# Kernel tuning notes

Hardware: AMD Instinct MI355X
Metric: run time of the kernel (lower is better)

Reference implementation:

```python
import jax, jax.numpy as jnp
import numpy as np

D_MODEL = 1024
N_HEADS = 16
N_KV_HEADS = 4
HEAD_DIM = 64


def setup_inputs() -> dict:
    key = jax.random.key(0)
    ks = jax.random.split(key, 5)
    B, T, P = 2, 512, 8
    scale = 1.0 / np.sqrt(D_MODEL)
    return {
        "hidden_states": jax.random.normal(ks[0], (B, T, P, D_MODEL), dtype=jnp.float32),
        # weights stored [in, out] so y = x @ W (same math as nn.Linear with W^T)
        "Wq": jax.random.normal(ks[1], (D_MODEL, N_HEADS * HEAD_DIM), dtype=jnp.float32) * scale,
        "Wk": jax.random.normal(ks[2], (D_MODEL, N_KV_HEADS * HEAD_DIM), dtype=jnp.float32) * scale,
        "Wv": jax.random.normal(ks[3], (D_MODEL, N_KV_HEADS * HEAD_DIM), dtype=jnp.float32) * scale,
        "Wo": jax.random.normal(ks[4], (N_HEADS * HEAD_DIM, D_MODEL), dtype=jnp.float32) * scale,
    }


def _rope_tables(T, d):
    half = d // 2
    inv_freq = 1.0 / (10000.0 ** (jnp.arange(half, dtype=jnp.float32) / half))
    pos = jnp.arange(T, dtype=jnp.float32)
    angles = pos[:, None] * inv_freq[None, :]  # (T, half)
    return jnp.cos(angles), jnp.sin(angles)


def _apply_rope(x, cos, sin):
    # x: (B, P, T, H, d); cos/sin: (T, d/2)
    half = x.shape[-1] // 2
    x1, x2 = x[..., :half], x[..., half:]
    c = cos[None, None, :, None, :]
    s = sin[None, None, :, None, :]
    return jnp.concatenate([x1 * c - x2 * s, x1 * s + x2 * c], axis=-1)


def reference(hidden_states, Wq, Wk, Wv, Wo):
    B, T, P, _ = hidden_states.shape
    x = jnp.transpose(hidden_states, (0, 2, 1, 3))  # (B, P, T, C)
    q = (x @ Wq).reshape(B, P, T, N_HEADS, HEAD_DIM)
    k = (x @ Wk).reshape(B, P, T, N_KV_HEADS, HEAD_DIM)
    v = (x @ Wv).reshape(B, P, T, N_KV_HEADS, HEAD_DIM)

    rep = N_HEADS // N_KV_HEADS
    k = jnp.repeat(k, rep, axis=3)  # (B,P,T,H,d) interleaved like torch repeat/view
    v = jnp.repeat(v, rep, axis=3)

    cos, sin = _rope_tables(T, HEAD_DIM)
    q = _apply_rope(q, cos, sin)
    k = _apply_rope(k, cos, sin)

    # (B,P,H,T,d)
    q = jnp.transpose(q, (0, 1, 3, 2, 4))
    k = jnp.transpose(k, (0, 1, 3, 2, 4))
    v = jnp.transpose(v, (0, 1, 3, 2, 4))

    attn = jnp.einsum("bphqd,bphkd->bphqk", q, k) / jnp.sqrt(
        jnp.asarray(HEAD_DIM, q.dtype))
    attn = jax.nn.softmax(attn, axis=-1)
    out = jnp.einsum("bphqk,bphkd->bphqd", attn, v)
    out = jnp.transpose(out, (0, 1, 3, 2, 4)).reshape(B, P, T, N_HEADS * HEAD_DIM)
    out = jnp.transpose(out, (0, 2, 1, 3))  # (B, T, P, H*d)
    return out @ Wo
```

## Files before the change

kernel.cpp:

```cpp
#include <hip/hip_runtime.h>
#include <stdint.h>


typedef __attribute__((ext_vector_type(8))) short bf16x8;
typedef __attribute__((ext_vector_type(4))) float f32x4;
typedef __attribute__((ext_vector_type(16))) float f32x16;
typedef __attribute__((ext_vector_type(4))) unsigned short us4;
typedef __attribute__((ext_vector_type(8))) unsigned short us8;

static __device__ __forceinline__ unsigned short f2bf(float f) {
  unsigned u = __float_as_uint(f);
  u += 0x7fffu + ((u >> 16) & 1u);
  return (unsigned short)(u >> 16);
}

static __device__ __forceinline__ void ld_lds16(const void* g, void* l) {
  __builtin_amdgcn_global_load_lds(
      (const __attribute__((address_space(1))) void*)g,
      (__attribute__((address_space(3))) void*)l, 16, 0, 0);
}

static __device__ __forceinline__ f32x4 mfma16(bf16x8 a, bf16x8 b, f32x4 c) {
  return __builtin_amdgcn_mfma_f32_16x16x32_bf16(a, b, c, 0, 0, 0);
}
static __device__ __forceinline__ f32x16 mfma32(bf16x8 a, bf16x8 b, f32x16 c) {
  return __builtin_amdgcn_mfma_f32_32x32x16_bf16(a, b, c, 0, 0, 0);
}

__global__ __launch_bounds__(256) void conv_all(
    const float* __restrict__ hs, const float* __restrict__ Wq,
    const float* __restrict__ Wk, const float* __restrict__ Wv,
    const float* __restrict__ Wo, unsigned short* __restrict__ xb,
    unsigned short* __restrict__ wqkv, unsigned short* __restrict__ wot) {
  __shared__ float tile[64][65];
  int bid = blockIdx.x, tid = threadIdx.x;
  if (bid < 8192) {
    int gid = bid * 256 + tid;
    size_t e = (size_t)gid * 4;
    int r = (int)(e >> 10);
    int d = (int)(e & 1023);
    int b = r >> 12, p = (r >> 9) & 7, t = r & 511;
    const float4* src = (const float4*)(hs + ((((size_t)b * 512 + t) * 8 + p) << 10) + d);
    float4 v = *src;
    us4 o;
    o.x = f2bf(v.x); o.y = f2bf(v.y); o.z = f2bf(v.z); o.w = f2bf(v.w);
    *(us4*)(xb + e) = o;
    return;
  }
  int tb = bid - 8192;
  const float* W; unsigned short* Wt; int N, tc0, tn0;
  if (tb < 256)      { W = Wq; Wt = wqkv;                       N = 1024; tc0 = (tb >> 4) * 64;          tn0 = (tb & 15) * 64; }
  else if (tb < 320) { W = Wk; Wt = wqkv + (size_t)1024 * 1024; N = 256;  tc0 = ((tb - 256) >> 2) * 64;  tn0 = ((tb - 256) & 3) * 64; }
  else if (tb < 384) { W = Wv; Wt = wqkv + (size_t)1280 * 1024; N = 256;  tc0 = ((tb - 320) >> 2) * 64;  tn0 = ((tb - 320) & 3) * 64; }
  else               { W = Wo; Wt = wot;                        N = 1024; tc0 = ((tb - 384) >> 4) * 64;  tn0 = ((tb - 384) & 15) * 64; }
  int tr = tid >> 4, tc = tid & 15;
#pragma unroll
  for (int i = 0; i < 4; ++i) {
    int c = tr + i * 16;
    float4 v = *(const float4*)(W + (size_t)(tc0 + c) * N + tn0 + tc * 4);
    tile[c][tc * 4 + 0] = v.x; tile[c][tc * 4 + 1] = v.y;
    tile[c][tc * 4 + 2] = v.z; tile[c][tc * 4 + 3] = v.w;
  }
  __syncthreads();
#pragma unroll
  for (int i = 0; i < 4; ++i) {
    int n = tr + i * 16;
    us4 o;
    o.x = f2bf(tile[tc * 4 + 0][n]); o.y = f2bf(tile[tc * 4 + 1][n]);
    o.z = f2bf(tile[tc * 4 + 2][n]); o.w = f2bf(tile[tc * 4 + 3][n]);
    *(us4*)(Wt + (size_t)(tn0 + n) * 1024 + tc0 + tc * 4) = o;
  }
}

__global__ __launch_bounds__(512, 2) void gemm_qkv(
    const unsigned short* __restrict__ A, const unsigned short* __restrict__ Bt,
    unsigned short* __restrict__ qb, unsigned short* __restrict__ kb,
    unsigned short* __restrict__ vtb) {
  constexpr int K = 1024;
  constexpr int KT = K / 64;
  __shared__ __align__(16) unsigned short Sm[2][2][256 * 64];
  unsigned short* Cs = &Sm[0][0][0];

  int tid = threadIdx.x;
  int lane = tid & 63, wid = tid >> 6;
  int quad = lane >> 4, lo = lane & 15;
  int wg = (blockIdx.x & 7) * 24 + (blockIdx.x >> 3);
  int tn = wg % 6, tm = wg / 6;
  int wr = wid >> 2, wc = wid & 3;
  int srow = lane >> 3, schunk = lane & 7;
  int cg = schunk ^ srow;

  const unsigned short* pa = A + ((size_t)(tm * 256) + wid * 8 + srow) * K + cg * 8;
  const unsigned short* pb = Bt + ((size_t)(tn * 256) + wid * 8 + srow) * K + cg * 8;

  f32x4 z = {0.f, 0.f, 0.f, 0.f};
  f32x4 acc[8][4];
#pragma unroll
  for (int i = 0; i < 8; ++i)
#pragma unroll
    for (int j = 0; j < 4; ++j) acc[i][j] = z;

  auto stage = [&](int t, int p) {
#pragma unroll
    for (int i = 0; i < 4; ++i) {
      ld_lds16(pa + (size_t)i * 64 * K + t * 64,
               (char*)&Sm[p][0][0] + (wid * 8 + i * 64) * 128);
      ld_lds16(pb + (size_t)i * 64 * K + t * 64,
               (char*)&Sm[p][1][0] + (wid * 8 + i * 64) * 128);
    }
  };

  stage(0, 0);
  stage(1, 1);
  asm volatile("s_waitcnt vmcnt(8)" ::: "memory");
  asm volatile("s_barrier" ::: "memory");

  bf16x8 af[4][2], bb0[2][2], bb1[2][2];

  for (int t = 0; t < KT; ++t) {
    int p = t & 1;
    const unsigned short* As = &Sm[p][0][0];
    const unsigned short* Bs = &Sm[p][1][0];

#pragma unroll
    for (int mi = 0; mi < 4; ++mi)
#pragma unroll
      for (int kx = 0; kx < 2; ++kx) {
        int row = wr * 128 + mi * 16 + lo;
        int cgx = (quad + kx * 4) ^ (row & 7);
        af[mi][kx] = *(const bf16x8*)(As + (size_t)row * 64 + cgx * 8);
      }
#pragma unroll
    for (int ni = 0; ni < 2; ++ni)
#pragma unroll
      for (int kx = 0; kx < 2; ++kx) {
        int row = wc * 64 + ni * 16 + lo;
        int cgx = (quad + kx * 4) ^ (row & 7);
        bb0[ni][kx] = *(const bf16x8*)(Bs + (size_t)row * 64 + cgx * 8);
      }
    asm volatile("s_barrier" ::: "memory");
    __builtin_amdgcn_s_setprio(1);
#pragma unroll
    for (int kx = 0; kx < 2; ++kx)
#pragma unroll
      for (int mi = 0; mi < 4; ++mi)
#pragma unroll
        for (int ni = 0; ni < 2; ++ni)
          acc[mi][ni] = mfma16(af[mi][kx], bb0[ni][kx], acc[mi][ni]);
    __builtin_amdgcn_s_setprio(0);
    asm volatile("s_barrier" ::: "memory");

#pragma unroll
    for (int ni = 0; ni < 2; ++ni)
#pragma unroll
      for (int kx = 0; kx < 2; ++kx) {
        int row = wc * 64 + (ni + 2) * 16 + lo;
        int cgx = (quad + kx * 4) ^ (row & 7);
        bb1[ni][kx] = *(const bf16x8*)(Bs + (size_t)row * 64 + cgx * 8);
      }
    asm volatile("s_barrier" ::: "memory");
    __builtin_amdgcn_s_setprio(1);
#pragma unroll
    for (int kx = 0; kx < 2; ++kx)
#pragma unroll
      for (int mi = 0; mi < 4; ++mi)
#pragma unroll
        for (int ni = 0; ni < 2; ++ni)
          acc[mi][ni + 2] = mfma16(af[mi][kx], bb1[ni][kx], acc[mi][ni + 2]);
    __builtin_amdgcn_s_setprio(0);
    asm volatile("s_barrier" ::: "memory");

#pragma unroll
    for (int mi = 0; mi < 4; ++mi)
#pragma unroll
      for (int kx = 0; kx < 2; ++kx) {
        int row = wr * 128 + 64 + mi * 16 + lo;
        int cgx = (quad + kx * 4) ^ (row & 7);
        af[mi][kx] = *(const bf16x8*)(As + (size_t)row * 64 + cgx * 8);
      }
    asm volatile("s_barrier" ::: "memory");
    __builtin_amdgcn_s_setprio(1);
#pragma unroll
    for (int kx = 0; kx < 2; ++kx)
#pragma unroll
      for (int mi = 0; mi < 4; ++mi)
#pragma unroll
        for (int ni = 0; ni < 2; ++ni)
          acc[mi + 4][ni + 2] = mfma16(af[mi][kx], bb1[ni][kx], acc[mi + 4][ni + 2]);
    __builtin_amdgcn_s_setprio(0);
    asm volatile("s_barrier" ::: "memory");

    bool pf = (t + 2 < KT);
    if (pf) stage(t + 2, p);
    __builtin_amdgcn_s_setprio(1);
#pragma unroll
    for (int kx = 0; kx < 2; ++kx)
#pragma unroll
      for (int mi = 0; mi < 4; ++mi)
#pragma unroll
        for (int ni = 0; ni < 2; ++ni)
          acc[mi + 4][ni] = mfma16(af[mi][kx], bb0[ni][kx], acc[mi + 4][ni]);
    __builtin_amdgcn_s_setprio(0);
    if (pf) asm volatile("s_waitcnt vmcnt(8)" ::: "memory");
    else    asm volatile("s_waitcnt vmcnt(0)" ::: "memory");
    asm volatile("s_barrier" ::: "memory");
  }

  if (tn < 5) {
    float qscale = (tn < 4) ? 0.125f : 1.0f;
#pragma unroll
    for (int mi = 0; mi < 8; ++mi)
#pragma unroll
      for (int r = 0; r < 4; ++r) {
        int row = wr * 128 + mi * 16 + quad * 4 + r;
        int tpos = (tm * 256 + row) & 511;
#pragma unroll
        for (int ni = 0; ni < 2; ++ni) {
          float invf = exp2f((float)(ni * 16 + lo) * -0.41524101186092029f);
          float ang = (float)tpos * invf;
          float s, c;
          __sincosf(ang, &s, &c);
          float x1 = acc[mi][ni][r], x2 = acc[mi][ni + 2][r];
          acc[mi][ni][r]     = (x1 * c - x2 * s) * qscale;
          acc[mi][ni + 2][r] = (x1 * s + x2 * c) * qscale;
        }
      }
#pragma unroll
    for (int mi = 0; mi < 8; ++mi)
#pragma unroll
      for (int ni = 0; ni < 4; ++ni)
#pragma unroll
        for (int r = 0; r < 4; ++r) {
          int row = wr * 128 + mi * 16 + quad * 4 + r;
          int col = wc * 64 + ni * 16 + lo;
          int cs = col ^ (((row >> 2) & 3) << 3);
          Cs[row * 256 + cs] = f2bf(acc[mi][ni][r]);
        }
    __syncthreads();
    int tc = tid & 31, ro = tid >> 5;
#pragma unroll
    for (int it = 0; it < 16; ++it) {
      int row = ro + 16 * it;
      int cs = (tc * 8) ^ (((row >> 2) & 3) << 3);
      us8 v = *(const us8*)(Cs + row * 256 + cs);
      size_t grow = (size_t)(tm * 256 + row);
      if (tn < 4) *(us8*)(qb + grow * 1024 + tn * 256 + tc * 8) = v;
      else        *(us8*)(kb + grow * 256 + tc * 8) = v;
    }
  } else {
#pragma unroll
    for (int mi = 0; mi < 8; ++mi)
#pragma unroll
      for (int ni = 0; ni < 4; ++ni)
#pragma unroll
        for (int r = 0; r < 4; ++r) {
          int trow = wr * 128 + mi * 16 + quad * 4 + r;
          int col = wc * 64 + ni * 16 + lo;
          Cs[col * 256 + (trow ^ ((col & 7) << 3))] = f2bf(acc[mi][ni][r]);
        }
    __syncthreads();
    int t0 = (tid & 31) * 8, colIdx = tid >> 5;
    int bp = tm >> 1, tbase = (tm & 1) * 256;
#pragma unroll
    for (int it = 0; it < 16; ++it) {
      int col = colIdx + it * 16;
      us8 v = *(const us8*)(Cs + col * 256 + (t0 ^ ((col & 7) << 3)));
      int hh = col >> 6, dd = col & 63;
      *(us8*)(vtb + (((size_t)(bp * 4 + hh)) * 64 + dd) * 512 + tbase + t0) = v;
    }
  }
}

__global__ __launch_bounds__(512, 2) void gemm_o(
    const unsigned short* __restrict__ A, const unsigned short* __restrict__ Bt,
    float* __restrict__ out) {
  constexpr int K = 1024;
  constexpr int KT = K / 64;
  __shared__ __align__(16) unsigned short Sm[2][(128 + 256) * 64];

  int tid = threadIdx.x;
  int lane = tid & 63, wid = tid >> 6;
  int quad = lane >> 4, lo = lane & 15;
  int wg = (blockIdx.x & 7) * 32 + (blockIdx.x >> 3);
  int tn = wg & 3, tm = wg >> 2;
  int wr = wid >> 2, wc = wid & 3;
  int srow = lane >> 3, schunk = lane & 7;
  int cg = schunk ^ srow;

  const unsigned short* pa = A + ((size_t)(tm * 128) + wid * 8 + srow) * K + cg * 8;
  const unsigned short* pb = Bt + ((size_t)(tn * 256) + wid * 8 + srow) * K + cg * 8;

  f32x4 z = {0.f, 0.f, 0.f, 0.f};
  f32x4 acc[4][4];
#pragma unroll
  for (int i = 0; i < 4; ++i)
#pragma unroll
    for (int j = 0; j < 4; ++j) acc[i][j] = z;

  auto stage = [&](int t, int p) {
    unsigned short* As = &Sm[p][0];
    unsigned short* Bs = &Sm[p][128 * 64];
#pragma unroll
    for (int i = 0; i < 2; ++i)
      ld_lds16(pa + (size_t)i * 64 * K + t * 64,
               (char*)As + (wid * 8 + i * 64) * 128);
#pragma unroll
    for (int i = 0; i < 4; ++i)
      ld_lds16(pb + (size_t)i * 64 * K + t * 64,
               (char*)Bs + (wid * 8 + i * 64) * 128);
  };

  stage(0, 0);
  stage(1, 1);
  asm volatile("s_waitcnt vmcnt(6)" ::: "memory");
  asm volatile("s_barrier" ::: "memory");

  bf16x8 af[4][2], bb0[2][2], bb1[2][2];

  for (int t = 0; t < KT; ++t) {
    int p = t & 1;
    const unsigned short* As = &Sm[p][0];
    const unsigned short* Bs = &Sm[p][128 * 64];

#pragma unroll
    for (int mi = 0; mi < 4; ++mi)
#pragma unroll
      for (int kx = 0; kx < 2; ++kx) {
        int row = wr * 64 + mi * 16 + lo;
        int cgx = (quad + kx * 4) ^ (row & 7);
        af[mi][kx] = *(const bf16x8*)(As + (size_t)row * 64 + cgx * 8);
      }
#pragma unroll
    for (int ni = 0; ni < 2; ++ni)
#pragma unroll
      for (int kx = 0; kx < 2; ++kx) {
        int row = wc * 64 + ni * 16 + lo;
        int cgx = (quad + kx * 4) ^ (row & 7);
        bb0[ni][kx] = *(const bf16x8*)(Bs + (size_t)row * 64 + cgx * 8);
      }
#pragma unroll
    for (int ni = 0; ni < 2; ++ni)
#pragma unroll
      for (int kx = 0; kx < 2; ++kx) {
        int row = wc * 64 + (ni + 2) * 16 + lo;
        int cgx = (quad + kx * 4) ^ (row & 7);
        bb1[ni][kx] = *(const bf16x8*)(Bs + (size_t)row * 64 + cgx * 8);
      }
    asm volatile("s_barrier" ::: "memory");
    __builtin_amdgcn_s_setprio(1);
#pragma unroll
    for (int kx = 0; kx < 2; ++kx)
#pragma unroll
      for (int mi = 0; mi < 4; ++mi)
#pragma unroll
        for (int ni = 0; ni < 2; ++ni)
          acc[mi][ni] = mfma16(af[mi][kx], bb0[ni][kx], acc[mi][ni]);
    __builtin_amdgcn_s_setprio(0);
    asm volatile("s_barrier" ::: "memory");

    bool pf = (t + 2 < KT);
    if (pf) stage(t + 2, p);
    __builtin_amdgcn_s_setprio(1);
#pragma unroll
    for (int kx = 0; kx < 2; ++kx)
#pragma unroll
      for (int mi = 0; mi < 4; ++mi)
#pragma unroll
        for (int ni = 0; ni < 2; ++ni)
          acc[mi][ni + 2] = mfma16(af[mi][kx], bb1[ni][kx], acc[mi][ni + 2]);
    __builtin_amdgcn_s_setprio(0);
    if (pf) asm volatile("s_waitcnt vmcnt(6)" ::: "memory");
    else    asm volatile("s_waitcnt vmcnt(0)" ::: "memory");
    asm volatile("s_barrier" ::: "memory");
  }

#pragma unroll
  for (int mi = 0; mi < 4; ++mi) {
    for (int ni = 0; ni < 4; ++ni) {
      int col = tn * 256 + wc * 64 + ni * 16 + lo;
      for (int r = 0; r < 4; ++r) {
        int grow = tm * 128 + wr * 64 + mi * 16 + quad * 4 + r;
        int bp = grow >> 9, tt = grow & 511;
        int b = bp >> 3, pp = bp & 7;
        out[((((size_t)b * 512 + tt) * 8 + pp) << 10) + col] = acc[mi][ni][r];
      }
    }
  }
}

__global__ __launch_bounds__(512, 2) void attn(
    const unsigned short* __restrict__ qbuf, const unsigned short* __restrict__ kb,
    const unsigned short* __restrict__ vtb, unsigned short* __restrict__ ao) {
  __shared__ __align__(16) unsigned short Ks[2][64 * 64];
  __shared__ __align__(16) unsigned short Vs[2][64 * 64];

  int tid = threadIdx.x;
  int lane = tid & 63, wid = tid >> 6;
  int lo32 = lane & 31, hl = lane >> 5;
  int wg = (blockIdx.x & 7) * 32 + (blockIdx.x >> 3);
  int head = wg & 15, bp = wg >> 4;
  int kvh = head >> 2;
  int srow = lane >> 3, schunk = lane & 7;

  const unsigned short* kg = kb + ((size_t)bp * 512) * 256 + kvh * 64;
  const unsigned short* vg = vtb + ((size_t)(bp * 4 + kvh)) * 64 * 512;

  const unsigned short* qgA =
      qbuf + ((size_t)(bp * 512 + wid * 64 + lo32)) * 1024 + head * 64;
  bf16x8 qA[4], qB[4];
#pragma unroll
  for (int kkc = 0; kkc < 4; ++kkc) {
    int ch = 2 * kkc + hl;
    qA[kkc] = *(const bf16x8*)(qgA + ch * 8);
    qB[kkc] = *(const bf16x8*)(qgA + (size_t)32 * 1024 + ch * 8);
  }

  auto stageKV = [&](int kt, int p) {
    int row = wid * 8 + srow;
    int cg = schunk ^ (row & 7);
    ld_lds16(kg + (size_t)(kt * 64 + row) * 256 + cg * 8,
             (char*)&Ks[p][0] + (wid * 8) * 128);
    ld_lds16(vg + (size_t)row * 512 + kt * 64 + cg * 8,
             (char*)&Vs[p][0] + (wid * 8) * 128);
  };

  stageKV(0, 0);
  stageKV(1, 1);
  asm volatile("s_waitcnt vmcnt(2)" ::: "memory");
  asm volatile("s_barrier" ::: "memory");

  f32x16 z16 = {0.f};
  f32x16 oA0 = z16, oA1 = z16, oB0 = z16, oB1 = z16;
  float psumA = 0.f, psumB = 0.f;

  for (int kt = 0; kt < 8; ++kt) {
    int p = kt & 1;
    const unsigned short* Kp = &Ks[p][0];
    const unsigned short* Vp = &Vs[p][0];

    f32x16 sA0 = z16, sA1 = z16, sB0 = z16, sB1 = z16;
#pragma unroll
    for (int kkc = 0; kkc < 4; ++kkc) {
      int ch = 2 * kkc + hl;
      bf16x8 kf0 = *(const bf16x8*)(Kp + (size_t)lo32 * 64 + ((ch ^ (lo32 & 7)) * 8));
      bf16x8 kf1 = *(const bf16x8*)(Kp + (size_t)(32 + lo32) * 64 + ((ch ^ (lo32 & 7)) * 8));
      sA0 = mfma32(kf0, qA[kkc], sA0);
      sA1 = mfma32(kf1, qA[kkc], sA1);
      sB0 = mfma32(kf0, qB[kkc], sB0);
      sB1 = mfma32(kf1, qB[kkc], sB1);
    }

#pragma unroll
    for (int t = 0; t < 2; ++t) {
      const f32x16& svA = t ? sA1 : sA0;
      const f32x16& svB = t ? sB1 : sB0;
      unsigned pkA[8], xpA[8], pkB[8], xpB[8];
#pragma unroll
      for (int pp = 0; pp < 8; ++pp) {
        float a0 = __expf(svA[2 * pp]);
        float a1 = __expf(svA[2 * pp + 1]);
        psumA += a0 + a1;
        pkA[pp] = ((__float_as_uint(a0) + 0x8000u) >> 16) |
                  ((__float_as_uint(a1) + 0x8000u) & 0xffff0000u);
        float b0 = __expf(svB[2 * pp]);
        float b1 = __expf(svB[2 * pp + 1]);
        psumB += b0 + b1;
        pkB[pp] = ((__float_as_uint(b0) + 0x8000u) >> 16) |
                  ((__float_as_uint(b1) + 0x8000u) & 0xffff0000u);
      }
#pragma unroll
      for (int pp = 0; pp < 8; ++pp) {
        xpA[pp] = (unsigned)__shfl_xor((int)pkA[pp], 32);
        xpB[pp] = (unsigned)__shfl_xor((int)pkB[pp], 32);
      }
#pragma unroll
      for (int cc = 0; cc < 2; ++cc) {
        int o = cc * 4;
        union { unsigned u[4]; bf16x8 v; } fA, fB;
        if (hl == 0) {
          fA.u[0] = pkA[o];     fA.u[1] = pkA[o + 1];
          fA.u[2] = xpA[o];     fA.u[3] = xpA[o + 1];
          fB.u[0] = pkB[o];     fB.u[1] = pkB[o + 1];
          fB.u[2] = xpB[o];     fB.u[3] = xpB[o + 1];
        } else {
          fA.u[0] = xpA[o + 2]; fA.u[1] = xpA[o + 3];
          fA.u[2] = pkA[o + 2]; fA.u[3] = pkA[o + 3];
          fB.u[0] = xpB[o + 2]; fB.u[1] = xpB[o + 3];
          fB.u[2] = pkB[o + 2]; fB.u[3] = pkB[o + 3];
        }
        int vch = 2 * (t * 2 + cc) + hl;
        bf16x8 v0 = *(const bf16x8*)(Vp + (size_t)lo32 * 64 + ((vch ^ (lo32 & 7)) * 8));
        bf16x8 v1 = *(const bf16x8*)(Vp + (size_t)(32 + lo32) * 64 + ((vch ^ (lo32 & 7)) * 8));
        oA0 = mfma32(fA.v, v0, oA0);
        oA1 = mfma32(fA.v, v1, oA1);
        oB0 = mfma32(fB.v, v0, oB0);
        oB1 = mfma32(fB.v, v1, oB1);
      }
    }

    if (kt == 7) break;
    asm volatile("s_barrier" ::: "memory");
    if (kt < 6) {
      stageKV(kt + 2, p);
      asm volatile("s_waitcnt vmcnt(2)" ::: "memory");
    } else {
      asm volatile("s_waitcnt vmcnt(0)" ::: "memory");
    }
    asm volatile("s_barrier" ::: "memory");
  }

  psumA += __shfl_xor(psumA, 32);
  psumB += __shfl_xor(psumB, 32);
  float invA = 1.f / psumA, invB = 1.f / psumB;
#pragma unroll
  for (int r = 0; r < 16; ++r) {
    int q_r = (r & 3) + 8 * (r >> 2) + 4 * hl;
    float scA = __shfl(invA, q_r);
    float scB = __shfl(invB, q_r);
    size_t gA = (size_t)(bp * 512 + wid * 64 + q_r);
    ao[gA * 1024 + head * 64 + lo32]      = f2bf(oA0[r] * scA);
    ao[gA * 1024 + head * 64 + 32 + lo32] = f2bf(oA1[r] * scA);
    size_t gB = gA + 32;
    ao[gB * 1024 + head * 64 + lo32]      = f2bf(oB0[r] * scB);
    ao[gB * 1024 + head * 64 + 32 + lo32] = f2bf(oB1[r] * scB);
  }
}

extern "C" void kernel_launch(void* const* d_in, const int* in_sizes, int n_in,
                              void* d_out, int out_size, void* d_ws, size_t ws_size,
                              hipStream_t stream) {
  const float* hs = (const float*)d_in[0];
  const float* Wq = (const float*)d_in[1];
  const float* Wk = (const float*)d_in[2];
  const float* Wv = (const float*)d_in[3];
  const float* Wo = (const float*)d_in[4];
  float* out = (float*)d_out;

  unsigned short* xb   = (unsigned short*)d_ws;
  unsigned short* wqkv = xb + (size_t)8192 * 1024;
  unsigned short* wot  = wqkv + (size_t)1536 * 1024;
  unsigned short* qbuf = wot + (size_t)1024 * 1024;
  unsigned short* kbuf = qbuf + (size_t)8192 * 1024;
  unsigned short* vtb  = kbuf + (size_t)8192 * 256;
  unsigned short* ao   = xb;

  conv_all<<<8832, 256, 0, stream>>>(hs, Wq, Wk, Wv, Wo, xb, wqkv, wot);
  gemm_qkv<<<192, 512, 0, stream>>>(xb, wqkv, qbuf, kbuf, vtb);
  attn<<<256, 512, 0, stream>>>(qbuf, kbuf, vtb, ao);
  gemm_o<<<256, 512, 0, stream>>>(ao, wot, out);
}
```

Baseline: 176.7 us.

## Retile QKV GEMM to 128x384 tiles with interleaved RoPE weight layout

Changes the QKV projection GEMM from 256x256 tiles on 192 blocks to 128x384 tiles on 256 blocks, so the grid covers all CUs more evenly. The Q and K weight columns are permuted during conversion so RoPE pairs land in adjacent columns. The rotation is then done with a lane shuffle instead of pairing accumulator tiles. This adds more epilogue branching, and the mixed K/V tile in the last column group needs split write paths, with less A-tile reuse per block.

```diff
diff --git a/kernel.cpp b/kernel.cpp
--- a/kernel.cpp
+++ b/kernel.cpp
@@ -53,6 +53,7 @@
   else if (tb < 320) { W = Wk; Wt = wqkv + (size_t)1024 * 1024; N = 256;  tc0 = ((tb - 256) >> 2) * 64;  tn0 = ((tb - 256) & 3) * 64; }
   else if (tb < 384) { W = Wv; Wt = wqkv + (size_t)1280 * 1024; N = 256;  tc0 = ((tb - 320) >> 2) * 64;  tn0 = ((tb - 320) & 3) * 64; }
   else               { W = Wo; Wt = wot;                        N = 1024; tc0 = ((tb - 384) >> 4) * 64;  tn0 = ((tb - 384) & 15) * 64; }
+  bool il = (tb < 320);
   int tr = tid >> 4, tc = tid & 15;
 #pragma unroll
   for (int i = 0; i < 4; ++i) {
@@ -68,7 +69,8 @@
     us4 o;
     o.x = f2bf(tile[tc * 4 + 0][n]); o.y = f2bf(tile[tc * 4 + 1][n]);
     o.z = f2bf(tile[tc * 4 + 2][n]); o.w = f2bf(tile[tc * 4 + 3][n]);
-    *(us4*)(Wt + (size_t)(tn0 + n) * 1024 + tc0 + tc * 4) = o;
+    int p = il ? ((n < 32) ? n * 2 : (n - 32) * 2 + 1) : n;
+    *(us4*)(Wt + (size_t)(tn0 + p) * 1024 + tc0 + tc * 4) = o;
   }
 }
 
@@ -78,36 +80,37 @@
     unsigned short* __restrict__ vtb) {
   constexpr int K = 1024;
   constexpr int KT = K / 64;
-  __shared__ __align__(16) unsigned short Sm[2][2][256 * 64];
-  unsigned short* Cs = &Sm[0][0][0];
+  __shared__ __align__(16) unsigned short Sm[2][(128 + 384) * 64];
+  unsigned short* Cs = &Sm[0][0];
 
   int tid = threadIdx.x;
   int lane = tid & 63, wid = tid >> 6;
   int quad = lane >> 4, lo = lane & 15;
-  int wg = (blockIdx.x & 7) * 24 + (blockIdx.x >> 3);
-  int tn = wg % 6, tm = wg / 6;
+  int wg = (blockIdx.x & 7) * 32 + (blockIdx.x >> 3);
+  int tn = wg & 3, tm = wg >> 2;
   int wr = wid >> 2, wc = wid & 3;
   int srow = lane >> 3, schunk = lane & 7;
   int cg = schunk ^ srow;
 
-  const unsigned short* pa = A + ((size_t)(tm * 256) + wid * 8 + srow) * K + cg * 8;
-  const unsigned short* pb = Bt + ((size_t)(tn * 256) + wid * 8 + srow) * K + cg * 8;
+  const unsigned short* pa = A + ((size_t)(tm * 128) + wid * 8 + srow) * K + cg * 8;
+  const unsigned short* pb = Bt + ((size_t)(tn * 384) + wid * 8 + srow) * K + cg * 8;
 
   f32x4 z = {0.f, 0.f, 0.f, 0.f};
-  f32x4 acc[8][4];
-#pragma unroll
-  for (int i = 0; i < 8; ++i)
-#pragma unroll
-    for (int j = 0; j < 4; ++j) acc[i][j] = z;
+  f32x4 acc[4][6];
+#pragma unroll
+  for (int i = 0; i < 4; ++i)
+#pragma unroll
+    for (int j = 0; j < 6; ++j) acc[i][j] = z;
 
   auto stage = [&](int t, int p) {
-#pragma unroll
-    for (int i = 0; i < 4; ++i) {
-      ld_lds16(pa + (size_t)i * 64 * K + t * 64,
-               (char*)&Sm[p][0][0] + (wid * 8 + i * 64) * 128);
-      ld_lds16(pb + (size_t)i * 64 * K + t * 64,
-               (char*)&Sm[p][1][0] + (wid * 8 + i * 64) * 128);
-    }
+    unsigned short* As_ = &Sm[p][0];
+    unsigned short* Bs_ = &Sm[p][128 * 64];
+#pragma unroll
+    for (int i = 0; i < 2; ++i)
+      ld_lds16(pa + (size_t)i * 64 * K + t * 64, (char*)As_ + (wid * 8 + i * 64) * 128);
+#pragma unroll
+    for (int i = 0; i < 6; ++i)
+      ld_lds16(pb + (size_t)i * 64 * K + t * 64, (char*)Bs_ + (wid * 8 + i * 64) * 128);
   };
 
   stage(0, 0);
@@ -115,28 +118,28 @@
   asm volatile("s_waitcnt vmcnt(8)" ::: "memory");
   asm volatile("s_barrier" ::: "memory");
 
-  bf16x8 af[4][2], bb0[2][2], bb1[2][2];
+  bf16x8 af[4][2], bb[3][2];
 
   for (int t = 0; t < KT; ++t) {
     int p = t & 1;
-    const unsigned short* As = &Sm[p][0][0];
-    const unsigned short* Bs = &Sm[p][1][0];
+    const unsigned short* As = &Sm[p][0];
+    const unsigned short* Bs = &Sm[p][128 * 64];
 
 #pragma unroll
     for (int mi = 0; mi < 4; ++mi)
 #pragma unroll
       for (int kx = 0; kx < 2; ++kx) {
-        int row = wr * 128 + mi * 16 + lo;
+        int row = wr * 64 + mi * 16 + lo;
         int cgx = (quad + kx * 4) ^ (row & 7);
         af[mi][kx] = *(const bf16x8*)(As + (size_t)row * 64 + cgx * 8);
       }
 #pragma unroll
-    for (int ni = 0; ni < 2; ++ni)
+    for (int ni = 0; ni < 3; ++ni)
 #pragma unroll
       for (int kx = 0; kx < 2; ++kx) {
-        int row = wc * 64 + ni * 16 + lo;
+        int row = wc * 96 + ni * 16 + lo;
         int cgx = (quad + kx * 4) ^ (row & 7);
-        bb0[ni][kx] = *(const bf16x8*)(Bs + (size_t)row * 64 + cgx * 8);
+        bb[ni][kx] = *(const bf16x8*)(Bs + (size_t)row * 64 + cgx * 8);
       }
     asm volatile("s_barrier" ::: "memory");
     __builtin_amdgcn_s_setprio(1);
@@ -145,51 +148,22 @@
 #pragma unroll
       for (int mi = 0; mi < 4; ++mi)
 #pragma unroll
-        for (int ni = 0; ni < 2; ++ni)
-          acc[mi][ni] = mfma16(af[mi][kx], bb0[ni][kx], acc[mi][ni]);
+        for (int ni = 0; ni < 3; ++ni)
+          acc[mi][ni] = mfma16(af[mi][kx], bb[ni][kx], acc[mi][ni]);
     __builtin_amdgcn_s_setprio(0);
     asm volatile("s_barrier" ::: "memory");
 
 #pragma unroll
-    for (int ni = 0; ni < 2; ++ni)
+    for (int ni = 0; ni < 3; ++ni)
 #pragma unroll
       for (int kx = 0; kx < 2; ++kx) {
-        int row = wc * 64 + (ni + 2) * 16 + lo;
+        int row = wc * 96 + (ni + 3) * 16 + lo;
         int cgx = (quad + kx * 4) ^ (row & 7);
-        bb1[ni][kx] = *(const bf16x8*)(Bs + (size_t)row * 64 + cgx * 8);
-      }
-    asm volatile("s_barrier" ::: "memory");
-    __builtin_amdgcn_s_setprio(1);
-#pragma unroll
-    for (int kx = 0; kx < 2; ++kx)
-#pragma unroll
-      for (int mi = 0; mi < 4; ++mi)
-#pragma unroll
-        for (int ni = 0; ni < 2; ++ni)
-          acc[mi][ni + 2] = mfma16(af[mi][kx], bb1[ni][kx], acc[mi][ni + 2]);
-    __builtin_amdgcn_s_setprio(0);
-    asm volatile("s_barrier" ::: "memory");
-
-#pragma unroll
-    for (int mi = 0; mi < 4; ++mi)
-#pragma unroll
-      for (int kx = 0; kx < 2; ++kx) {
-        int row = wr * 128 + 64 + mi * 16 + lo;
-        int cgx = (quad + kx * 4) ^ (row & 7);
-        af[mi][kx] = *(const bf16x8*)(As + (size_t)row * 64 + cgx * 8);
-      }
-    asm volatile("s_barrier" ::: "memory");
-    __builtin_amdgcn_s_setprio(1);
-#pragma unroll
-    for (int kx = 0; kx < 2; ++kx)
-#pragma unroll
-      for (int mi = 0; mi < 4; ++mi)
-#pragma unroll
-        for (int ni = 0; ni < 2; ++ni)
-          acc[mi + 4][ni + 2] = mfma16(af[mi][kx], bb1[ni][kx], acc[mi + 4][ni + 2]);
-    __builtin_amdgcn_s_setprio(0);
-    asm volatile("s_barrier" ::: "memory");
-
+        bb[ni][kx] = *(const bf16x8*)(Bs + (size_t)row * 64 + cgx * 8);
+      }
+    asm volatile("s_waitcnt lgkmcnt(0)" ::: "memory");
+    __builtin_amdgcn_sched_barrier(0);
+    asm volatile("s_barrier" ::: "memory");
     bool pf = (t + 2 < KT);
     if (pf) stage(t + 2, p);
     __builtin_amdgcn_s_setprio(1);
@@ -198,73 +172,83 @@
 #pragma unroll
       for (int mi = 0; mi < 4; ++mi)
 #pragma unroll
-        for (int ni = 0; ni < 2; ++ni)
-          acc[mi + 4][ni] = mfma16(af[mi][kx], bb0[ni][kx], acc[mi + 4][ni]);
+        for (int ni = 0; ni < 3; ++ni)
+          acc[mi][ni + 3] = mfma16(af[mi][kx], bb[ni][kx], acc[mi][ni + 3]);
     __builtin_amdgcn_s_setprio(0);
     if (pf) asm volatile("s_waitcnt vmcnt(8)" ::: "memory");
     else    asm volatile("s_waitcnt vmcnt(0)" ::: "memory");
     asm volatile("s_barrier" ::: "memory");
   }
-
-  if (tn < 5) {
-    float qscale = (tn < 4) ? 0.125f : 1.0f;
-#pragma unroll
-    for (int mi = 0; mi < 8; ++mi)
-#pragma unroll
-      for (int r = 0; r < 4; ++r) {
-        int row = wr * 128 + mi * 16 + quad * 4 + r;
-        int tpos = (tm * 256 + row) & 511;
-#pragma unroll
-        for (int ni = 0; ni < 2; ++ni) {
-          float invf = exp2f((float)(ni * 16 + lo) * -0.41524101186092029f);
+  __syncthreads();
+
+  int Ws = (tn == 3) ? 128 : 384;
+  unsigned short* Cv = Cs + 128 * 128;
+  float sgn = (lane & 1) ? 1.f : -1.f;
+#pragma unroll
+  for (int ni = 0; ni < 6; ++ni) {
+    int colb = wc * 96 + ni * 16;
+    int blkg = tn * 6 + (colb >> 6);
+    if (blkg < 20) {
+      float qs = (blkg < 16) ? 0.125f : 1.0f;
+      int kidx = ((colb & 63) + lo) >> 1;
+      float invf = exp2f((float)kidx * -0.41524101186092029f);
+      int col = colb + lo;
+#pragma unroll
+      for (int mi = 0; mi < 4; ++mi)
+#pragma unroll
+        for (int r = 0; r < 4; ++r) {
+          int row = wr * 64 + mi * 16 + quad * 4 + r;
+          int tpos = (tm * 128 + row) & 511;
           float ang = (float)tpos * invf;
           float s, c;
           __sincosf(ang, &s, &c);
-          float x1 = acc[mi][ni][r], x2 = acc[mi][ni + 2][r];
-          acc[mi][ni][r]     = (x1 * c - x2 * s) * qscale;
-          acc[mi][ni + 2][r] = (x1 * s + x2 * c) * qscale;
+          float x = acc[mi][ni][r];
+          float xo = __shfl_xor(x, 1);
+          float out = (x * c + sgn * xo * s) * qs;
+          Cs[row * Ws + (col ^ (((row >> 2) & 3) << 3))] = f2bf(out);
         }
-      }
-#pragma unroll
-    for (int mi = 0; mi < 8; ++mi)
-#pragma unroll
-      for (int ni = 0; ni < 4; ++ni)
+    } else {
+      int cv = colb + lo - 128;
+#pragma unroll
+      for (int mi = 0; mi < 4; ++mi)
 #pragma unroll
         for (int r = 0; r < 4; ++r) {
-          int row = wr * 128 + mi * 16 + quad * 4 + r;
-          int col = wc * 64 + ni * 16 + lo;
-          int cs = col ^ (((row >> 2) & 3) << 3);
-          Cs[row * 256 + cs] = f2bf(acc[mi][ni][r]);
+          int trow = wr * 64 + mi * 16 + quad * 4 + r;
+          Cv[cv * 128 + (trow ^ ((cv & 7) << 3))] = f2bf(acc[mi][ni][r]);
         }
-    __syncthreads();
-    int tc = tid & 31, ro = tid >> 5;
-#pragma unroll
-    for (int it = 0; it < 16; ++it) {
-      int row = ro + 16 * it;
-      int cs = (tc * 8) ^ (((row >> 2) & 3) << 3);
-      us8 v = *(const us8*)(Cs + row * 256 + cs);
-      size_t grow = (size_t)(tm * 256 + row);
-      if (tn < 4) *(us8*)(qb + grow * 1024 + tn * 256 + tc * 8) = v;
-      else        *(us8*)(kb + grow * 256 + tc * 8) = v;
+    }
+  }
+  __syncthreads();
+
+  if (tn < 3) {
+#pragma unroll
+    for (int it = 0; it < 12; ++it) {
+      int linear = it * 512 + tid;
+      int row = linear / 48, ch = linear % 48;
+      int cs = (ch * 8) ^ (((row >> 2) & 3) << 3);
+      us8 v = *(const us8*)(Cs + row * 384 + cs);
+      int g = tn * 384 + ch * 8;
+      size_t grow = (size_t)(tm * 128 + row);
+      if (g < 1024) *(us8*)(qb + grow * 1024 + g) = v;
+      else          *(us8*)(kb + grow * 256 + (g - 1024)) = v;
     }
   } else {
 #pragma unroll
-    for (int mi = 0; mi < 8; ++mi)
-#pragma unroll
-      for (int ni = 0; ni < 4; ++ni)
-#pragma unroll
-        for (int r = 0; r < 4; ++r) {
-          int trow = wr * 128 + mi * 16 + quad * 4 + r;
-          int col = wc * 64 + ni * 16 + lo;
-          Cs[col * 256 + (trow ^ ((col & 7) << 3))] = f2bf(acc[mi][ni][r]);
-        }
-    __syncthreads();
-    int t0 = (tid & 31) * 8, colIdx = tid >> 5;
-    int bp = tm >> 1, tbase = (tm & 1) * 256;
-#pragma unroll
-    for (int it = 0; it < 16; ++it) {
-      int col = colIdx + it * 16;
-      us8 v = *(const us8*)(Cs + col * 256 + (t0 ^ ((col & 7) << 3)));
+    for (int it = 0; it < 4; ++it) {
+      int linear = it * 512 + tid;
+      int row = linear >> 4, ch = linear & 15;
+      int cs = (ch * 8) ^ (((row >> 2) & 3) << 3);
+      us8 v = *(const us8*)(Cs + row * 128 + cs);
+      size_t grow = (size_t)(tm * 128 + row);
+      *(us8*)(kb + grow * 256 + 128 + ch * 8) = v;
+    }
+    int chunk = tid & 15, colIdx = tid >> 4;
+    int bp = tm >> 2, tbase = (tm & 3) * 128;
+#pragma unroll
+    for (int it = 0; it < 8; ++it) {
+      int col = colIdx + 32 * it;
+      int t0 = chunk * 8;
+      us8 v = *(const us8*)(Cv + col * 128 + (t0 ^ ((col & 7) << 3)));
       int hh = col >> 6, dd = col & 63;
       *(us8*)(vtb + (((size_t)(bp * 4 + hh)) * 64 + dd) * 512 + tbase + t0) = v;
     }
@@ -545,7 +529,7 @@
   unsigned short* ao   = xb;
 
   conv_all<<<8832, 256, 0, stream>>>(hs, Wq, Wk, Wv, Wo, xb, wqkv, wot);
-  gemm_qkv<<<192, 512, 0, stream>>>(xb, wqkv, qbuf, kbuf, vtb);
+  gemm_qkv<<<256, 512, 0, stream>>>(xb, wqkv, qbuf, kbuf, vtb);
   attn<<<256, 512, 0, stream>>>(qbuf, kbuf, vtb, ao);
   gemm_o<<<256, 512, 0, stream>>>(ao, wot, out);
 }
```

Result: no change. 175.1 us (-0.9%).
